# Performance work log

Measured on AMD Instinct MI355X. Metric: run time of the kernel, lower is better.

Reference implementation:

```python
import jax, jax.numpy as jnp
import numpy as np

SIGMA = 1.0          # config.rendering.sigma
EPS = 1e-8
GRID_RES = 64
N_QUERY = 16384
N_VOXELS = 8192      # max_voxels // 4
FEAT_DIM = 4


def setup_inputs() -> dict:
    key = jax.random.key(0)
    k1, k2, k3 = jax.random.split(key, 3)
    # query points live in the grid coordinate space [0, GRID_RES)
    query_points = jax.random.uniform(k1, (N_QUERY, 3), jnp.float32) * GRID_RES
    # voxel coords are integer grid coordinates stored as float (as in torch init)
    voxel_coords = jax.random.randint(k2, (N_VOXELS, 3), 0, GRID_RES).astype(jnp.float32)
    voxel_features = jax.random.normal(k3, (N_VOXELS, FEAT_DIM), jnp.float32) * 0.01
    voxel_sizes = jnp.ones((N_VOXELS,), jnp.float32)  # voxel_size = 1.0
    return {
        "query_points": query_points,
        "voxel_coords": voxel_coords,
        "voxel_features": voxel_features,
        "voxel_sizes": voxel_sizes,
    }


def reference(query_points, voxel_coords, voxel_features, voxel_sizes):
    # Euclidean cdist via the |q|^2 + |c|^2 - 2 q.c expansion (GEMM-friendly)
    q2 = jnp.sum(query_points * query_points, axis=-1, keepdims=True)        # [N,1]
    c2 = jnp.sum(voxel_coords * voxel_coords, axis=-1)                        # [M]
    d2 = q2 + c2[None, :] - 2.0 * (query_points @ voxel_coords.T)             # [N,M]
    distances = jnp.sqrt(jnp.maximum(d2, 0.0))
    # RBF-style kernel + row normalization (soft rasterization branch)
    weights = jnp.exp(-distances / (2.0 * SIGMA ** 2))                        # [N,M]
    weights = weights / (jnp.sum(weights, axis=1, keepdims=True) + EPS)
    # weighted feature / size interpolation
    feats = weights @ voxel_features                                          # [N,4]
    sizes = weights @ voxel_sizes                                             # [N]
    densities = jax.nn.softplus(feats[:, 0])                                  # [N]
    colors = jax.nn.sigmoid(feats[:, 1:4])                                    # [N,3]
    return densities, colors, sizes, weights
```

## Files before the change

kernel.cpp:

```cpp
#include <hip/hip_runtime.h>
#include <cmath>

#define N_QUERY 16384
#define N_VOX   8192
#define Q_ROWS  4
#define BLOCK   512
#define NGROUP  4

typedef float f32x4 __attribute__((ext_vector_type(4)));

#if __has_builtin(__builtin_amdgcn_exp2f)
__device__ __forceinline__ float fast_exp2(float x) { return __builtin_amdgcn_exp2f(x); }
#else
__device__ __forceinline__ float fast_exp2(float x) { float r; asm("v_exp_f32 %0, %1" : "=v"(r) : "v"(x)); return r; }
#endif

#if __has_builtin(__builtin_amdgcn_sqrtf)
__device__ __forceinline__ float fast_sqrt(float x) { return __builtin_amdgcn_sqrtf(x); }
#else
__device__ __forceinline__ float fast_sqrt(float x) { float r; asm("v_sqrt_f32 %0, %1" : "=v"(r) : "v"(x)); return r; }
#endif

__device__ __forceinline__ float wave_reduce_sum(float v) {
    #pragma unroll
    for (int off = 32; off > 0; off >>= 1) v += __shfl_xor(v, off, 64);
    return v;
}

#define NEG_HALF_LOG2E (-0.7213475204444817f)

__global__ __launch_bounds__(BLOCK, 2)
void voxel_interp_kernel(const float* __restrict__ qp,
                         const float* __restrict__ vc,
                         const float* __restrict__ vf,
                         const float* __restrict__ vs,
                         float* __restrict__ dens,
                         float* __restrict__ cols,
                         float* __restrict__ sizes,
                         float* __restrict__ wout)
{
    const int t = threadIdx.x;
    const int rowbase = blockIdx.x * Q_ROWS;

    float qx[Q_ROWS], qy[Q_ROWS], qz[Q_ROWS];
    #pragma unroll
    for (int q = 0; q < Q_ROWS; ++q) {
        qx[q] = qp[(rowbase + q) * 3 + 0];
        qy[q] = qp[(rowbase + q) * 3 + 1];
        qz[q] = qp[(rowbase + q) * 3 + 2];
    }

    float asum[Q_ROWS], af0[Q_ROWS], af1[Q_ROWS], af2[Q_ROWS], af3[Q_ROWS], asz[Q_ROWS];
    #pragma unroll
    for (int q = 0; q < Q_ROWS; ++q) {
        asum[q] = 0.f; af0[q] = 0.f; af1[q] = 0.f; af2[q] = 0.f; af3[q] = 0.f; asz[q] = 0.f;
    }

    #pragma unroll
    for (int g = 0; g < NGROUP; ++g) {
        const int v0 = g * (N_VOX / NGROUP) + t * 4;
        const float4* cp = reinterpret_cast<const float4*>(vc + (size_t)v0 * 3);
        float4 c0 = cp[0], c1 = cp[1], c2 = cp[2];
        float cxs[4] = {c0.x, c0.w, c1.z, c2.y};
        float cys[4] = {c0.y, c1.x, c1.w, c2.z};
        float czs[4] = {c0.z, c1.y, c2.x, c2.w};
        const float4* fp = reinterpret_cast<const float4*>(vf + (size_t)v0 * 4);
        float4 fa[4] = {fp[0], fp[1], fp[2], fp[3]};
        float4 sz4 = *reinterpret_cast<const float4*>(vs + v0);
        float szs[4] = {sz4.x, sz4.y, sz4.z, sz4.w};

        #pragma unroll
        for (int i = 0; i < 4; ++i) {
            const float cx = cxs[i], cy = cys[i], cz = czs[i];
            #pragma unroll
            for (int q = 0; q < Q_ROWS; ++q) {
                float dx = qx[q] - cx;
                float dy = qy[q] - cy;
                float dz = qz[q] - cz;
                float d2 = dx * dx + dy * dy + dz * dz;
                float ww = fast_exp2(fast_sqrt(d2) * NEG_HALF_LOG2E);
                asum[q] += ww;
                af0[q] += ww * fa[i].x;
                af1[q] += ww * fa[i].y;
                af2[q] += ww * fa[i].z;
                af3[q] += ww * szs[i] * 0.0f + ww * fa[i].w;
                asz[q] += ww * szs[i];
            }
        }
    }

    float vals[Q_ROWS * 6];
    #pragma unroll
    for (int q = 0; q < Q_ROWS; ++q) {
        vals[q * 6 + 0] = asum[q];
        vals[q * 6 + 1] = af0[q];
        vals[q * 6 + 2] = af1[q];
        vals[q * 6 + 3] = af2[q];
        vals[q * 6 + 4] = af3[q];
        vals[q * 6 + 5] = asz[q];
    }

    __shared__ float red[BLOCK / 64][Q_ROWS * 6];
    __shared__ float fin[Q_ROWS * 6];
    const int wave = t >> 6;
    const int lane = t & 63;
    #pragma unroll
    for (int i = 0; i < Q_ROWS * 6; ++i) {
        float r = wave_reduce_sum(vals[i]);
        if (lane == 0) red[wave][i] = r;
    }
    __syncthreads();
    if (t < Q_ROWS * 6) {
        float s = 0.f;
        #pragma unroll
        for (int wv = 0; wv < BLOCK / 64; ++wv) s += red[wv][t];
        fin[t] = s;
    }
    __syncthreads();

    float inv[Q_ROWS];
    #pragma unroll
    for (int q = 0; q < Q_ROWS; ++q) {
        inv[q] = 1.0f / (fin[q * 6 + 0] + 1e-8f);
    }

    #pragma unroll
    for (int g = 0; g < NGROUP; ++g) {
        const int v0 = g * (N_VOX / NGROUP) + t * 4;
        const float4* cp = reinterpret_cast<const float4*>(vc + (size_t)v0 * 3);
        float4 c0 = cp[0], c1 = cp[1], c2 = cp[2];
        float cxs[4] = {c0.x, c0.w, c1.z, c2.y};
        float cys[4] = {c0.y, c1.x, c1.w, c2.z};
        float czs[4] = {c0.z, c1.y, c2.x, c2.w};

        #pragma unroll
        for (int q = 0; q < Q_ROWS; ++q) {
            const float iv = inv[q];
            f32x4 o;
            #pragma unroll
            for (int i = 0; i < 4; ++i) {
                float dx = qx[q] - cxs[i];
                float dy = qy[q] - cys[i];
                float dz = qz[q] - czs[i];
                float d2 = dx * dx + dy * dy + dz * dz;
                float ww = fast_exp2(fast_sqrt(d2) * NEG_HALF_LOG2E);
                o[i] = ww * iv;
            }
            float* base = wout + (size_t)(rowbase + q) * N_VOX;
            __builtin_nontemporal_store(o, reinterpret_cast<f32x4*>(base + v0));
        }
    }

    if (t < Q_ROWS) {
        const int q = t;
        const int row = rowbase + q;
        const float iv = inv[q];
        const float f0 = fin[q * 6 + 1] * iv;
        const float f1 = fin[q * 6 + 2] * iv;
        const float f2 = fin[q * 6 + 3] * iv;
        const float f3 = fin[q * 6 + 4] * iv;
        const float sz = fin[q * 6 + 5] * iv;
        dens[row] = log1pf(expf(f0));
        cols[row * 3 + 0] = 1.0f / (1.0f + expf(-f1));
        cols[row * 3 + 1] = 1.0f / (1.0f + expf(-f2));
        cols[row * 3 + 2] = 1.0f / (1.0f + expf(-f3));
        sizes[row] = sz;
    }
}

extern "C" void kernel_launch(void* const* d_in, const int* in_sizes, int n_in,
                              void* d_out, int out_size, void* d_ws, size_t ws_size,
                              hipStream_t stream) {
    const float* qp = (const float*)d_in[0];
    const float* vc = (const float*)d_in[1];
    const float* vf = (const float*)d_in[2];
    const float* vs = (const float*)d_in[3];

    float* out   = (float*)d_out;
    float* dens  = out;
    float* cols  = out + N_QUERY;
    float* sizes = out + N_QUERY * 4;
    float* wout  = out + N_QUERY * 5;

    dim3 grid(N_QUERY / Q_ROWS);
    voxel_interp_kernel<<<grid, BLOCK, 0, stream>>>(qp, vc, vf, vs, dens, cols, sizes, wout);
}
```

Measured before the change: 226.6 us.

## Split fused kernel into row-sum kernel and separate weight-write kernel

The single kernel that computed row sums and then rewrote every weight is split in two. The first kernel computes the normalizers and outputs for 8 query rows per block and stores the inverse sums in workspace. The second kernel tiles 64 rows by 1024 voxels, recomputes the weights, and writes them with ordinary rather than nontemporal stores. This is meant to let the 512MB weight write run as a streaming, well-occupied kernel separate from the compute-heavy reduction, at the cost of a second launch and extra workspace traffic.

```diff
diff --git a/kernel.cpp b/kernel.cpp
--- a/kernel.cpp
+++ b/kernel.cpp
@@ -3,9 +3,15 @@
 
 #define N_QUERY 16384
 #define N_VOX   8192
-#define Q_ROWS  4
-#define BLOCK   512
-#define NGROUP  4
+
+#define A_BLOCK  512
+#define A_QROWS  8
+#define A_NGROUP 4
+
+#define B_BLOCK  256
+#define B_SEG    1024
+#define B_NSEG   (N_VOX / B_SEG)
+#define B_ROWS   64
 
 typedef float f32x4 __attribute__((ext_vector_type(4)));
 
@@ -29,36 +35,36 @@
 
 #define NEG_HALF_LOG2E (-0.7213475204444817f)
 
-__global__ __launch_bounds__(BLOCK, 2)
-void voxel_interp_kernel(const float* __restrict__ qp,
-                         const float* __restrict__ vc,
-                         const float* __restrict__ vf,
-                         const float* __restrict__ vs,
-                         float* __restrict__ dens,
-                         float* __restrict__ cols,
-                         float* __restrict__ sizes,
-                         float* __restrict__ wout)
+__global__ __launch_bounds__(A_BLOCK, 2)
+void sums_kernel(const float* __restrict__ qp,
+                 const float* __restrict__ vc,
+                 const float* __restrict__ vf,
+                 const float* __restrict__ vs,
+                 float* __restrict__ dens,
+                 float* __restrict__ cols,
+                 float* __restrict__ sizes,
+                 float* __restrict__ inv_ws)
 {
     const int t = threadIdx.x;
-    const int rowbase = blockIdx.x * Q_ROWS;
-
-    float qx[Q_ROWS], qy[Q_ROWS], qz[Q_ROWS];
-    #pragma unroll
-    for (int q = 0; q < Q_ROWS; ++q) {
+    const int rowbase = blockIdx.x * A_QROWS;
+
+    float qx[A_QROWS], qy[A_QROWS], qz[A_QROWS];
+    #pragma unroll
+    for (int q = 0; q < A_QROWS; ++q) {
         qx[q] = qp[(rowbase + q) * 3 + 0];
         qy[q] = qp[(rowbase + q) * 3 + 1];
         qz[q] = qp[(rowbase + q) * 3 + 2];
     }
 
-    float asum[Q_ROWS], af0[Q_ROWS], af1[Q_ROWS], af2[Q_ROWS], af3[Q_ROWS], asz[Q_ROWS];
-    #pragma unroll
-    for (int q = 0; q < Q_ROWS; ++q) {
+    float asum[A_QROWS], af0[A_QROWS], af1[A_QROWS], af2[A_QROWS], af3[A_QROWS], asz[A_QROWS];
+    #pragma unroll
+    for (int q = 0; q < A_QROWS; ++q) {
         asum[q] = 0.f; af0[q] = 0.f; af1[q] = 0.f; af2[q] = 0.f; af3[q] = 0.f; asz[q] = 0.f;
     }
 
     #pragma unroll
-    for (int g = 0; g < NGROUP; ++g) {
-        const int v0 = g * (N_VOX / NGROUP) + t * 4;
+    for (int g = 0; g < A_NGROUP; ++g) {
+        const int v0 = g * (N_VOX / A_NGROUP) + t * 4;
         const float4* cp = reinterpret_cast<const float4*>(vc + (size_t)v0 * 3);
         float4 c0 = cp[0], c1 = cp[1], c2 = cp[2];
         float cxs[4] = {c0.x, c0.w, c1.z, c2.y};
@@ -73,7 +79,7 @@
         for (int i = 0; i < 4; ++i) {
             const float cx = cxs[i], cy = cys[i], cz = czs[i];
             #pragma unroll
-            for (int q = 0; q < Q_ROWS; ++q) {
+            for (int q = 0; q < A_QROWS; ++q) {
                 float dx = qx[q] - cx;
                 float dy = qy[q] - cy;
                 float dz = qz[q] - cz;
@@ -83,15 +89,15 @@
                 af0[q] += ww * fa[i].x;
                 af1[q] += ww * fa[i].y;
                 af2[q] += ww * fa[i].z;
-                af3[q] += ww * szs[i] * 0.0f + ww * fa[i].w;
+                af3[q] += ww * fa[i].w;
                 asz[q] += ww * szs[i];
             }
         }
     }
 
-    float vals[Q_ROWS * 6];
-    #pragma unroll
-    for (int q = 0; q < Q_ROWS; ++q) {
+    float vals[A_QROWS * 6];
+    #pragma unroll
+    for (int q = 0; q < A_QROWS; ++q) {
         vals[q * 6 + 0] = asum[q];
         vals[q * 6 + 1] = af0[q];
         vals[q * 6 + 2] = af1[q];
@@ -100,71 +106,79 @@
         vals[q * 6 + 5] = asz[q];
     }
 
-    __shared__ float red[BLOCK / 64][Q_ROWS * 6];
-    __shared__ float fin[Q_ROWS * 6];
+    __shared__ float red[A_BLOCK / 64][A_QROWS * 6];
+    __shared__ float fin[A_QROWS * 6];
     const int wave = t >> 6;
     const int lane = t & 63;
     #pragma unroll
-    for (int i = 0; i < Q_ROWS * 6; ++i) {
+    for (int i = 0; i < A_QROWS * 6; ++i) {
         float r = wave_reduce_sum(vals[i]);
         if (lane == 0) red[wave][i] = r;
     }
     __syncthreads();
-    if (t < Q_ROWS * 6) {
+    if (t < A_QROWS * 6) {
         float s = 0.f;
         #pragma unroll
-        for (int wv = 0; wv < BLOCK / 64; ++wv) s += red[wv][t];
+        for (int wv = 0; wv < A_BLOCK / 64; ++wv) s += red[wv][t];
         fin[t] = s;
     }
     __syncthreads();
 
-    float inv[Q_ROWS];
-    #pragma unroll
-    for (int q = 0; q < Q_ROWS; ++q) {
-        inv[q] = 1.0f / (fin[q * 6 + 0] + 1e-8f);
-    }
-
-    #pragma unroll
-    for (int g = 0; g < NGROUP; ++g) {
-        const int v0 = g * (N_VOX / NGROUP) + t * 4;
-        const float4* cp = reinterpret_cast<const float4*>(vc + (size_t)v0 * 3);
-        float4 c0 = cp[0], c1 = cp[1], c2 = cp[2];
-        float cxs[4] = {c0.x, c0.w, c1.z, c2.y};
-        float cys[4] = {c0.y, c1.x, c1.w, c2.z};
-        float czs[4] = {c0.z, c1.y, c2.x, c2.w};
-
-        #pragma unroll
-        for (int q = 0; q < Q_ROWS; ++q) {
-            const float iv = inv[q];
-            f32x4 o;
-            #pragma unroll
-            for (int i = 0; i < 4; ++i) {
-                float dx = qx[q] - cxs[i];
-                float dy = qy[q] - cys[i];
-                float dz = qz[q] - czs[i];
-                float d2 = dx * dx + dy * dy + dz * dz;
-                float ww = fast_exp2(fast_sqrt(d2) * NEG_HALF_LOG2E);
-                o[i] = ww * iv;
-            }
-            float* base = wout + (size_t)(rowbase + q) * N_VOX;
-            __builtin_nontemporal_store(o, reinterpret_cast<f32x4*>(base + v0));
-        }
-    }
-
-    if (t < Q_ROWS) {
+    if (t < A_QROWS) {
         const int q = t;
         const int row = rowbase + q;
-        const float iv = inv[q];
+        const float iv = 1.0f / (fin[q * 6 + 0] + 1e-8f);
         const float f0 = fin[q * 6 + 1] * iv;
         const float f1 = fin[q * 6 + 2] * iv;
         const float f2 = fin[q * 6 + 3] * iv;
         const float f3 = fin[q * 6 + 4] * iv;
         const float sz = fin[q * 6 + 5] * iv;
+        inv_ws[row] = iv;
         dens[row] = log1pf(expf(f0));
         cols[row * 3 + 0] = 1.0f / (1.0f + expf(-f1));
         cols[row * 3 + 1] = 1.0f / (1.0f + expf(-f2));
         cols[row * 3 + 2] = 1.0f / (1.0f + expf(-f3));
         sizes[row] = sz;
+    }
+}
+
+__global__ __launch_bounds__(B_BLOCK)
+void weights_kernel(const float* __restrict__ qp,
+                    const float* __restrict__ vc,
+                    const float* __restrict__ inv_ws,
+                    float* __restrict__ wout)
+{
+    const int t = threadIdx.x;
+    const int seg = blockIdx.x % B_NSEG;
+    const int rowtile = blockIdx.x / B_NSEG;
+    const int rowbase = rowtile * B_ROWS;
+
+    const int v0 = seg * B_SEG + t * 4;
+    const float4* cp = reinterpret_cast<const float4*>(vc + (size_t)v0 * 3);
+    float4 c0 = cp[0], c1 = cp[1], c2 = cp[2];
+    const float cxs[4] = {c0.x, c0.w, c1.z, c2.y};
+    const float cys[4] = {c0.y, c1.x, c1.w, c2.z};
+    const float czs[4] = {c0.z, c1.y, c2.x, c2.w};
+
+    #pragma unroll 2
+    for (int r = 0; r < B_ROWS; ++r) {
+        const int row = rowbase + r;
+        const float qx = qp[row * 3 + 0];
+        const float qy = qp[row * 3 + 1];
+        const float qz = qp[row * 3 + 2];
+        const float iv = inv_ws[row];
+
+        f32x4 o;
+        #pragma unroll
+        for (int i = 0; i < 4; ++i) {
+            float dx = qx - cxs[i];
+            float dy = qy - cys[i];
+            float dz = qz - czs[i];
+            float d2 = dx * dx + dy * dy + dz * dz;
+            float ww = fast_exp2(fast_sqrt(d2) * NEG_HALF_LOG2E);
+            o[i] = ww * iv;
+        }
+        *reinterpret_cast<f32x4*>(wout + (size_t)row * N_VOX + v0) = o;
     }
 }
 
@@ -181,7 +195,11 @@
     float* cols  = out + N_QUERY;
     float* sizes = out + N_QUERY * 4;
     float* wout  = out + N_QUERY * 5;
-
-    dim3 grid(N_QUERY / Q_ROWS);
-    voxel_interp_kernel<<<grid, BLOCK, 0, stream>>>(qp, vc, vf, vs, dens, cols, sizes, wout);
-}
+    float* inv_ws = (float*)d_ws;
+
+    sums_kernel<<<dim3(N_QUERY / A_QROWS), A_BLOCK, 0, stream>>>(
+        qp, vc, vf, vs, dens, cols, sizes, inv_ws);
+
+    weights_kernel<<<dim3(B_NSEG * (N_QUERY / B_ROWS)), B_BLOCK, 0, stream>>>(
+        qp, vc, inv_ws, wout);
+}
```

Result: slower. 259.6 us (+14.6%).
